# Optimization experiments

Hardware: AMD Instinct MI355X
Metric: run time of the kernel (lower is better)

The kernel has to match this reference:

```python
import jax, jax.numpy as jnp
import numpy as np
import itertools

# Buffers from init_kwargs (constants)
N_GRID = (64, 64, 64)
GRID_MIN = 0.0
DX = 1.0 / 64.0
D, H, W = N_GRID[0] + 2, N_GRID[1] + 2, N_GRID[2] + 2  # padded grid 66^3


def setup_inputs() -> dict:
    key = jax.random.key(0)
    k1, k2, k3, k4 = jax.random.split(key, 4)
    B, N, Ci, Co = 2, 200000, 32, 32
    x = jax.random.normal(k1, (B, N, Ci), jnp.float32)
    # positions uniform in [0,1) -> Xp=(pos-grid_min)/dx in [0,64), indices in [0,65]
    pos = jax.random.uniform(k2, (B, N, 3), jnp.float32)
    kernel = jax.random.normal(k3, (3, 3, 3, Ci, Co), jnp.float32) * 0.1
    bias = jax.random.normal(k4, (Co,), jnp.float32) * 0.1
    return {"x": x, "pos": pos, "kernel": kernel, "bias": bias}


def _forward(x, pos, kernel, bias):
    B, N, Ci = x.shape
    Co = kernel.shape[-1]
    Xp = (pos - GRID_MIN) / DX                      # [B,N,3]
    base = Xp.astype(jnp.int32)                     # trunc == floor (Xp >= 0)
    fx = Xp - base.astype(Xp.dtype) - 0.5
    # quadratic B-spline weights: w[..., k, dim], k in {0,1,2}
    w = jnp.stack([0.5 * (0.5 - fx) ** 2,
                   0.75 - fx ** 2,
                   0.5 * (0.5 + fx) ** 2], axis=-2)  # [B,N,3,3]
    base = base + 1
    batch = jnp.arange(B)[:, None]                  # [B,1] for batched scatter
    result = jnp.zeros((B, D * H * W, Co), x.dtype)
    # 27 fixed stencil offsets (structural small loop, not a data-dim loop)
    for oi, oj, ok in itertools.product(range(3), repeat=3):
        weight = w[..., oi, 0] * w[..., oj, 1] * w[..., ok, 2]      # [B,N]
        idx = base + jnp.array([oi, oj, ok], jnp.int32) - 1          # [B,N,3]
        idx1d = idx[..., 0] * (H * W) + idx[..., 1] * W + idx[..., 2]
        vals = weight[..., None] * (x @ kernel[oi, oj, ok] + bias)   # [B,N,Co]
        result = result.at[batch, idx1d].add(vals)
    return result.reshape(B, D, H, W, Co).transpose(0, 4, 1, 2, 3)   # [B,Co,D,H,W]


def reference(x, pos, kernel, bias):
    return _forward(x, pos, kernel, bias)
```

## Files before the change

### kernel.cpp

```cpp
#include <hip/hip_runtime.h>

#define GD   66
#define GHW  (66*66)
#define GDHW (66*66*66)
#define CI   32
#define CO   32

__device__ __forceinline__ void atomAdd(float* p, float v) {
    unsafeAtomicAdd(p, v);
}

template<bool CELLCO>
__global__ __launch_bounds__(256) void p2g_kernel(
    const float* __restrict__ x, const float* __restrict__ pos,
    const float* __restrict__ kern, const float* __restrict__ bias,
    float* __restrict__ dst, int N, int nPairs)
{
    const int co   = threadIdx.x & 31;
    const int half = threadIdx.x >> 5;
    const float bco = bias[co];
    const int halvesTotal = gridDim.x * 8;

    for (int t = 0; t < 9; ++t) {
        const int oi = t / 3, oj = t - 3*oi;

        float kreg[3][32];
        #pragma unroll
        for (int ok = 0; ok < 3; ++ok) {
            const float* kp = kern + (size_t)(t*3 + ok)*1024 + co;
            #pragma unroll
            for (int ci = 0; ci < 32; ++ci)
                kreg[ok][ci] = kp[ci*32];
        }

        for (int pp = blockIdx.x*8 + half; pp < nPairs; pp += halvesTotal) {
            const int g0 = pp*2;

            float xr[2][32];
            #pragma unroll
            for (int p = 0; p < 2; ++p) {
                const float4* xp = (const float4*)(x + (size_t)(g0+p)*CI);
                #pragma unroll
                for (int i = 0; i < 8; ++i) {
                    float4 v = xp[i];
                    xr[p][4*i+0]=v.x; xr[p][4*i+1]=v.y; xr[p][4*i+2]=v.z; xr[p][4*i+3]=v.w;
                }
            }

            float wxy[2], wz[2][3];
            int cb[2], bsel[2];
            #pragma unroll
            for (int p = 0; p < 2; ++p) {
                const int gp = g0 + p;
                float px = pos[gp*3+0]*64.f, py = pos[gp*3+1]*64.f, pz = pos[gp*3+2]*64.f;
                int bx = (int)px, by = (int)py, bz = (int)pz;
                float fx = px - bx - 0.5f, fy = py - by - 0.5f, fz = pz - bz - 0.5f;
                float wx = (oi==0) ? 0.5f*(0.5f-fx)*(0.5f-fx)
                         : (oi==1) ? 0.75f - fx*fx
                                   : 0.5f*(0.5f+fx)*(0.5f+fx);
                float wy = (oj==0) ? 0.5f*(0.5f-fy)*(0.5f-fy)
                         : (oj==1) ? 0.75f - fy*fy
                                   : 0.5f*(0.5f+fy)*(0.5f+fy);
                wxy[p] = wx*wy;
                wz[p][0]=0.5f*(0.5f-fz)*(0.5f-fz); wz[p][1]=0.75f-fz*fz; wz[p][2]=0.5f*(0.5f+fz)*(0.5f+fz);
                cb[p]   = (bx+oi)*GHW + (by+oj)*GD + bz;
                bsel[p] = (gp >= N) ? 1 : 0;
            }

            float y[3][2];
            #pragma unroll
            for (int ok = 0; ok < 3; ++ok) { y[ok][0] = bco; y[ok][1] = bco; }
            #pragma unroll
            for (int ci = 0; ci < 32; ++ci) {
                float x0 = xr[0][ci], x1 = xr[1][ci];
                #pragma unroll
                for (int ok = 0; ok < 3; ++ok) {
                    float kv = kreg[ok][ci];
                    y[ok][0] += x0*kv;
                    y[ok][1] += x1*kv;
                }
            }

            #pragma unroll
            for (int ok = 0; ok < 3; ++ok) {
                {
                    int cell = cb[0] + ok;
                    size_t a = CELLCO ? (((size_t)bsel[0]*GDHW + cell)*32 + (size_t)co)
                                      : (((size_t)(bsel[0]*32 + co))*GDHW + (size_t)cell);
                    atomAdd(dst + a, wxy[0]*wz[0][ok]*y[ok][0]);
                }
                {
                    int cell = cb[1] + ok;
                    size_t a = CELLCO ? (((size_t)bsel[1]*GDHW + cell)*32 + (size_t)co)
                                      : (((size_t)(bsel[1]*32 + co))*GDHW + (size_t)cell);
                    atomAdd(dst + a, wxy[1]*wz[1][ok]*y[ok][1]);
                }
            }
        }
    }
}

__global__ __launch_bounds__(256) void transp_kernel(
    const float* __restrict__ ws, float* __restrict__ out)
{
    __shared__ float tile[32][33];
    const int b     = blockIdx.y;
    const int cell0 = blockIdx.x * 32;
    const int n     = min(32, GDHW - cell0);

    const float* src = ws + ((size_t)b*GDHW + cell0)*32;
    for (int e = threadIdx.x; e < n*32; e += 256)
        tile[e>>5][e&31] = src[e];
    __syncthreads();
    for (int e = threadIdx.x; e < 32*32; e += 256) {
        int c  = e >> 5;
        int cl = e & 31;
        if (cl < n)
            out[((size_t)(b*32 + c))*GDHW + cell0 + cl] = tile[cl][c];
    }
}

extern "C" void kernel_launch(void* const* d_in, const int* in_sizes, int n_in,
                              void* d_out, int out_size, void* d_ws, size_t ws_size,
                              hipStream_t stream) {
    const float* x    = (const float*)d_in[0];
    const float* pos  = (const float*)d_in[1];
    const float* kern = (const float*)d_in[2];
    const float* bias = (const float*)d_in[3];
    float* out = (float*)d_out;

    const int N  = in_sizes[0] / (2*CI);
    const int BN = 2*N;
    const int nPairs = (BN + 1) / 2;

    const size_t wsNeed = (size_t)2 * GDHW * CO * sizeof(float);

    if (ws_size >= wsNeed) {
        float* ws = (float*)d_ws;
        hipMemsetAsync(ws, 0, wsNeed, stream);
        p2g_kernel<true><<<dim3(2048), dim3(256), 0, stream>>>(x, pos, kern, bias, ws, N, nPairs);
        transp_kernel<<<dim3((GDHW + 31)/32, 2), dim3(256), 0, stream>>>(ws, out);
    } else {
        hipMemsetAsync(out, 0, (size_t)out_size * sizeof(float), stream);
        p2g_kernel<false><<<dim3(2048), dim3(256), 0, stream>>>(x, pos, kern, bias, out, N, nPairs);
    }
}
```

Before: 1.257 ms.

## Replace atomic scatter with bin-sort and atomic-free gather per output column

Particles are binned by cell with a histogram, a prefix scan and a reorder pass, storing features and spline weights contiguously. A gather kernel then computes each output (x,y) column by looping over the particles in its neighbouring bins, accumulating in registers and writing the channel-major output directly. This removes the float atomics and the separate transpose pass. The price is five extra small kernels, particle data being reread up to 27 times, and thread-divergent inner loops, since each bin holds roughly one particle.

```diff
diff --git a/kernel.cpp b/kernel.cpp
--- a/kernel.cpp
+++ b/kernel.cpp
@@ -5,13 +5,182 @@
 #define GDHW (66*66*66)
 #define CI   32
 #define CO   32
+#define NBINS (2*64*64*64)
+#define NSCAN_BLOCKS 2048
 
 __device__ __forceinline__ void atomAdd(float* p, float v) {
     unsafeAtomicAdd(p, v);
 }
 
-template<bool CELLCO>
-__global__ __launch_bounds__(256) void p2g_kernel(
+
+__global__ __launch_bounds__(256) void hist_kernel(
+    const float* __restrict__ pos, unsigned* __restrict__ counts,
+    unsigned* __restrict__ binA, unsigned* __restrict__ rankA,
+    int N, int total)
+{
+    int gp = blockIdx.x*256 + threadIdx.x;
+    if (gp >= total) return;
+    float px = pos[gp*3+0]*64.f, py = pos[gp*3+1]*64.f, pz = pos[gp*3+2]*64.f;
+    int bx = (int)px, by = (int)py, bz = (int)pz;
+    int b  = (gp >= N) ? 1 : 0;
+    unsigned bin = (((unsigned)(b*64 + bx))*64u + (unsigned)by)*64u + (unsigned)bz;
+    unsigned r = atomicAdd(&counts[bin], 1u);
+    binA[gp] = bin; rankA[gp] = r;
+}
+
+__global__ __launch_bounds__(256) void scan1_kernel(
+    const unsigned* __restrict__ counts, unsigned* __restrict__ offs,
+    unsigned* __restrict__ bsum)
+{
+    __shared__ unsigned ws[4];
+    int i = blockIdx.x*256 + threadIdx.x;
+    int lane = threadIdx.x & 63, wid = threadIdx.x >> 6;
+    unsigned v = counts[i], s = v;
+    #pragma unroll
+    for (int d = 1; d < 64; d <<= 1) { unsigned n = __shfl_up(s, d, 64); if (lane >= d) s += n; }
+    if (lane == 63) ws[wid] = s;
+    __syncthreads();
+    if (threadIdx.x == 0) {
+        unsigned r = 0;
+        for (int w = 0; w < 4; ++w) { unsigned t = ws[w]; ws[w] = r; r += t; }
+        bsum[blockIdx.x] = r;
+    }
+    __syncthreads();
+    offs[i] = ws[wid] + s - v;
+}
+
+__global__ __launch_bounds__(256) void scan2_kernel(unsigned* __restrict__ bsum)
+{
+    __shared__ unsigned ws[4];
+    __shared__ unsigned runsh;
+    if (threadIdx.x == 0) runsh = 0;
+    __syncthreads();
+    int lane = threadIdx.x & 63, wid = threadIdx.x >> 6;
+    for (int c = 0; c < NSCAN_BLOCKS; c += 256) {
+        unsigned v = bsum[c + threadIdx.x], s = v;
+        #pragma unroll
+        for (int d = 1; d < 64; d <<= 1) { unsigned n = __shfl_up(s, d, 64); if (lane >= d) s += n; }
+        if (lane == 63) ws[wid] = s;
+        __syncthreads();
+        unsigned run = runsh;
+        __syncthreads();
+        if (threadIdx.x == 0) {
+            unsigned r = 0;
+            for (int w = 0; w < 4; ++w) { unsigned t = ws[w]; ws[w] = r; r += t; }
+            runsh = run + r;
+        }
+        __syncthreads();
+        bsum[c + threadIdx.x] = run + ws[wid] + s - v;
+        __syncthreads();
+    }
+}
+
+__global__ __launch_bounds__(256) void scan3_kernel(
+    unsigned* __restrict__ offs, const unsigned* __restrict__ bsum, int total)
+{
+    int i = blockIdx.x*256 + threadIdx.x;
+    offs[i] += bsum[blockIdx.x];
+    if (i == 0) offs[NBINS] = (unsigned)total;
+}
+
+__global__ __launch_bounds__(256) void reorder_kernel(
+    const float* __restrict__ x, const float* __restrict__ pos,
+    const unsigned* __restrict__ offs, const unsigned* __restrict__ binA,
+    const unsigned* __restrict__ rankA,
+    float* __restrict__ X, float* __restrict__ W, int total)
+{
+    int gp = blockIdx.x*256 + threadIdx.x;
+    if (gp >= total) return;
+    unsigned dst = offs[binA[gp]] + rankA[gp];
+    const float4* xs = (const float4*)(x + (size_t)gp*32);
+    float4* xd = (float4*)(X + (size_t)dst*32);
+    #pragma unroll
+    for (int i = 0; i < 8; ++i) xd[i] = xs[i];
+    float px = pos[gp*3+0]*64.f, py = pos[gp*3+1]*64.f, pz = pos[gp*3+2]*64.f;
+    int bx = (int)px, by = (int)py, bz = (int)pz;
+    float fx = px-bx-0.5f, fy = py-by-0.5f, fz = pz-bz-0.5f;
+    float* w = W + (size_t)dst*9;
+    w[0]=0.5f*(0.5f-fx)*(0.5f-fx); w[1]=0.75f-fx*fx; w[2]=0.5f*(0.5f+fx)*(0.5f+fx);
+    w[3]=0.5f*(0.5f-fy)*(0.5f-fy); w[4]=0.75f-fy*fy; w[5]=0.5f*(0.5f+fy)*(0.5f+fy);
+    w[6]=0.5f*(0.5f-fz)*(0.5f-fz); w[7]=0.75f-fz*fz; w[8]=0.5f*(0.5f+fz)*(0.5f+fz);
+}
+
+__global__ __launch_bounds__(256) void gather_kernel(
+    const float* __restrict__ X, const float* __restrict__ W,
+    const unsigned* __restrict__ offs, const float* __restrict__ kern,
+    const float* __restrict__ bias, float* __restrict__ out)
+{
+    __shared__ float tile[GD][33];
+    const int bid = blockIdx.x;
+    const int b   = bid / (66*66);
+    const int rr  = bid % (66*66);
+    const int cx  = rr / 66, cy = rr % 66;
+    const int co   = threadIdx.x & 31;
+    const int half = threadIdx.x >> 5;
+    const float bco = bias[co];
+
+    float acc[9];
+    #pragma unroll
+    for (int k = 0; k < 9; ++k) acc[k] = 0.f;
+
+    for (int t = 0; t < 9; ++t) {
+        const int oi = t / 3, oj = t % 3;
+        const int gx = cx - oi, gy = cy - oj;
+        if ((unsigned)gx > 63u || (unsigned)gy > 63u) continue;
+
+        float kreg[3][32];
+        #pragma unroll
+        for (int ok = 0; ok < 3; ++ok) {
+            const float* kp = kern + (size_t)(t*3 + ok)*1024 + co;
+            #pragma unroll
+            for (int ci = 0; ci < 32; ++ci) kreg[ok][ci] = kp[ci*32];
+        }
+        const unsigned binbase = (((unsigned)(b*64 + gx))*64u + (unsigned)gy)*64u;
+
+        #pragma unroll
+        for (int k = 0; k < 9; ++k) {
+            const int cz = half + 8*k;
+            if (cz < GD) {
+                #pragma unroll
+                for (int ok = 0; ok < 3; ++ok) {
+                    const int gz = cz - ok;
+                    if ((unsigned)gz > 63u) continue;
+                    const unsigned bin = binbase + (unsigned)gz;
+                    const unsigned s = offs[bin], e = offs[bin+1];
+                    for (unsigned p = s; p < e; ++p) {
+                        const float4* xp = (const float4*)(X + (size_t)p*32);
+                        float xx[32];
+                        #pragma unroll
+                        for (int i = 0; i < 8; ++i) {
+                            float4 v = xp[i];
+                            xx[4*i+0]=v.x; xx[4*i+1]=v.y; xx[4*i+2]=v.z; xx[4*i+3]=v.w;
+                        }
+                        const float* wp = W + (size_t)p*9;
+                        float w = wp[oi]*wp[3+oj]*wp[6+ok];
+                        float dot = 0.f;
+                        #pragma unroll
+                        for (int ci = 0; ci < 32; ++ci) dot += xx[ci]*kreg[ok][ci];
+                        acc[k] += w*(dot + bco);
+                    }
+                }
+            }
+        }
+    }
+
+    #pragma unroll
+    for (int k = 0; k < 9; ++k) {
+        const int cz = half + 8*k;
+        if (cz < GD) tile[cz][co] = acc[k];
+    }
+    __syncthreads();
+    const size_t obase = (size_t)b*32*GDHW + (size_t)(cx*GHW + cy*GD);
+    for (int idx = threadIdx.x; idx < 32*GD; idx += 256) {
+        const int c2 = idx / GD, z2 = idx % GD;
+        out[obase + (size_t)c2*GDHW + z2] = tile[z2][c2];
+    }
+}
+
+__global__ __launch_bounds__(256) void p2g_fallback(
     const float* __restrict__ x, const float* __restrict__ pos,
     const float* __restrict__ kern, const float* __restrict__ bias,
     float* __restrict__ dst, int N, int nPairs)
@@ -23,19 +192,15 @@
 
     for (int t = 0; t < 9; ++t) {
         const int oi = t / 3, oj = t - 3*oi;
-
         float kreg[3][32];
         #pragma unroll
         for (int ok = 0; ok < 3; ++ok) {
             const float* kp = kern + (size_t)(t*3 + ok)*1024 + co;
             #pragma unroll
-            for (int ci = 0; ci < 32; ++ci)
-                kreg[ok][ci] = kp[ci*32];
-        }
-
+            for (int ci = 0; ci < 32; ++ci) kreg[ok][ci] = kp[ci*32];
+        }
         for (int pp = blockIdx.x*8 + half; pp < nPairs; pp += halvesTotal) {
             const int g0 = pp*2;
-
             float xr[2][32];
             #pragma unroll
             for (int p = 0; p < 2; ++p) {
@@ -46,27 +211,20 @@
                     xr[p][4*i+0]=v.x; xr[p][4*i+1]=v.y; xr[p][4*i+2]=v.z; xr[p][4*i+3]=v.w;
                 }
             }
-
-            float wxy[2], wz[2][3];
-            int cb[2], bsel[2];
+            float wxy[2], wz[2][3]; int cb[2], bsel[2];
             #pragma unroll
             for (int p = 0; p < 2; ++p) {
                 const int gp = g0 + p;
                 float px = pos[gp*3+0]*64.f, py = pos[gp*3+1]*64.f, pz = pos[gp*3+2]*64.f;
                 int bx = (int)px, by = (int)py, bz = (int)pz;
-                float fx = px - bx - 0.5f, fy = py - by - 0.5f, fz = pz - bz - 0.5f;
-                float wx = (oi==0) ? 0.5f*(0.5f-fx)*(0.5f-fx)
-                         : (oi==1) ? 0.75f - fx*fx
-                                   : 0.5f*(0.5f+fx)*(0.5f+fx);
-                float wy = (oj==0) ? 0.5f*(0.5f-fy)*(0.5f-fy)
-                         : (oj==1) ? 0.75f - fy*fy
-                                   : 0.5f*(0.5f+fy)*(0.5f+fy);
+                float fx = px-bx-0.5f, fy = py-by-0.5f, fz = pz-bz-0.5f;
+                float wx = (oi==0) ? 0.5f*(0.5f-fx)*(0.5f-fx) : (oi==1) ? 0.75f-fx*fx : 0.5f*(0.5f+fx)*(0.5f+fx);
+                float wy = (oj==0) ? 0.5f*(0.5f-fy)*(0.5f-fy) : (oj==1) ? 0.75f-fy*fy : 0.5f*(0.5f+fy)*(0.5f+fy);
                 wxy[p] = wx*wy;
                 wz[p][0]=0.5f*(0.5f-fz)*(0.5f-fz); wz[p][1]=0.75f-fz*fz; wz[p][2]=0.5f*(0.5f+fz)*(0.5f+fz);
                 cb[p]   = (bx+oi)*GHW + (by+oj)*GD + bz;
                 bsel[p] = (gp >= N) ? 1 : 0;
             }
-
             float y[3][2];
             #pragma unroll
             for (int ok = 0; ok < 3; ++ok) { y[ok][0] = bco; y[ok][1] = bco; }
@@ -76,47 +234,15 @@
                 #pragma unroll
                 for (int ok = 0; ok < 3; ++ok) {
                     float kv = kreg[ok][ci];
-                    y[ok][0] += x0*kv;
-                    y[ok][1] += x1*kv;
+                    y[ok][0] += x0*kv; y[ok][1] += x1*kv;
                 }
             }
-
             #pragma unroll
             for (int ok = 0; ok < 3; ++ok) {
-                {
-                    int cell = cb[0] + ok;
-                    size_t a = CELLCO ? (((size_t)bsel[0]*GDHW + cell)*32 + (size_t)co)
-                                      : (((size_t)(bsel[0]*32 + co))*GDHW + (size_t)cell);
-                    atomAdd(dst + a, wxy[0]*wz[0][ok]*y[ok][0]);
-                }
-                {
-                    int cell = cb[1] + ok;
-                    size_t a = CELLCO ? (((size_t)bsel[1]*GDHW + cell)*32 + (size_t)co)
-                                      : (((size_t)(bsel[1]*32 + co))*GDHW + (size_t)cell);
-                    atomAdd(dst + a, wxy[1]*wz[1][ok]*y[ok][1]);
-                }
-            }
-        }
-    }
-}
-
-__global__ __launch_bounds__(256) void transp_kernel(
-    const float* __restrict__ ws, float* __restrict__ out)
-{
-    __shared__ float tile[32][33];
-    const int b     = blockIdx.y;
-    const int cell0 = blockIdx.x * 32;
-    const int n     = min(32, GDHW - cell0);
-
-    const float* src = ws + ((size_t)b*GDHW + cell0)*32;
-    for (int e = threadIdx.x; e < n*32; e += 256)
-        tile[e>>5][e&31] = src[e];
-    __syncthreads();
-    for (int e = threadIdx.x; e < 32*32; e += 256) {
-        int c  = e >> 5;
-        int cl = e & 31;
-        if (cl < n)
-            out[((size_t)(b*32 + c))*GDHW + cell0 + cl] = tile[cl][c];
+                atomAdd(dst + ((size_t)(bsel[0]*32 + co))*GDHW + (size_t)(cb[0]+ok), wxy[0]*wz[0][ok]*y[ok][0]);
+                atomAdd(dst + ((size_t)(bsel[1]*32 + co))*GDHW + (size_t)(cb[1]+ok), wxy[1]*wz[1][ok]*y[ok][1]);
+            }
+        }
     }
 }
 
@@ -129,19 +255,39 @@
     const float* bias = (const float*)d_in[3];
     float* out = (float*)d_out;
 
-    const int N  = in_sizes[0] / (2*CI);
-    const int BN = 2*N;
-    const int nPairs = (BN + 1) / 2;
-
-    const size_t wsNeed = (size_t)2 * GDHW * CO * sizeof(float);
+    const int N     = in_sizes[0] / (2*CI);
+    const int total = 2*N;
+
+    const size_t offX    = 0;
+    const size_t offW    = offX + (size_t)total*32*4;
+    const size_t offCnt  = offW + (size_t)total*9*4;
+    const size_t offOffs = offCnt + (size_t)NBINS*4;
+    const size_t offBin  = (offOffs + (size_t)(NBINS+1)*4 + 255) & ~(size_t)255;
+    const size_t offRank = offBin + (size_t)total*4;
+    const size_t offBsum = offRank + (size_t)total*4;
+    const size_t wsNeed  = offBsum + (size_t)NSCAN_BLOCKS*4;
 
     if (ws_size >= wsNeed) {
-        float* ws = (float*)d_ws;
-        hipMemsetAsync(ws, 0, wsNeed, stream);
-        p2g_kernel<true><<<dim3(2048), dim3(256), 0, stream>>>(x, pos, kern, bias, ws, N, nPairs);
-        transp_kernel<<<dim3((GDHW + 31)/32, 2), dim3(256), 0, stream>>>(ws, out);
+        char* wsb = (char*)d_ws;
+        float*    X      = (float*)   (wsb + offX);
+        float*    W      = (float*)   (wsb + offW);
+        unsigned* counts = (unsigned*)(wsb + offCnt);
+        unsigned* offs   = (unsigned*)(wsb + offOffs);
+        unsigned* binA   = (unsigned*)(wsb + offBin);
+        unsigned* rankA  = (unsigned*)(wsb + offRank);
+        unsigned* bsum   = (unsigned*)(wsb + offBsum);
+
+        (void)hipMemsetAsync(counts, 0, (size_t)NBINS*4, stream);
+        const int pb = (total + 255)/256;
+        hist_kernel   <<<dim3(pb),           dim3(256), 0, stream>>>(pos, counts, binA, rankA, N, total);
+        scan1_kernel  <<<dim3(NSCAN_BLOCKS), dim3(256), 0, stream>>>(counts, offs, bsum);
+        scan2_kernel  <<<dim3(1),            dim3(256), 0, stream>>>(bsum);
+        scan3_kernel  <<<dim3(NSCAN_BLOCKS), dim3(256), 0, stream>>>(offs, bsum, total);
+        reorder_kernel<<<dim3(pb),           dim3(256), 0, stream>>>(x, pos, offs, binA, rankA, X, W, total);
+        gather_kernel <<<dim3(2*66*66),      dim3(256), 0, stream>>>(X, W, offs, kern, bias, out);
     } else {
-        hipMemsetAsync(out, 0, (size_t)out_size * sizeof(float), stream);
-        p2g_kernel<false><<<dim3(2048), dim3(256), 0, stream>>>(x, pos, kern, bias, out, N, nPairs);
-    }
-}
+        (void)hipMemsetAsync(out, 0, (size_t)out_size * sizeof(float), stream);
+        const int nPairs = (total + 1) / 2;
+        p2g_fallback<<<dim3(2048), dim3(256), 0, stream>>>(x, pos, kern, bias, out, N, nPairs);
+    }
+}
```

After: 3.222 ms. 156% more time.
